# Performance work log

Measured on AMD Instinct MI355X. Metric: run time of the kernel, lower is better.

## Reference

```python
import jax, jax.numpy as jnp
import numpy as np

POOL_LEN = 2
POOL_SIZE = 4  # pool_len**2
NUM_ITERS = 3

def pool_grid(pool_size):
    # grid of relative positions inside the pooling block, row-major, centered at 0
    b = int(np.sqrt(pool_size))
    off = np.arange(b, dtype=np.float32) - (b - 1) / 2.0
    hh, ww = np.meshgrid(off, off, indexing='ij')
    return jnp.asarray(np.stack([hh.ravel(), ww.ravel()], -1))  # (pool_size, 2)

def posevec_to_rotmat(p):
    # p = (cos t, sin t) unit vector -> [[c,-s],[s,c]]
    x, y = p[..., 0], p[..., 1]
    return jnp.stack([jnp.stack([x, -y], -1), jnp.stack([y, x], -1)], -2)

def inverse_pose(p):
    return jnp.stack([p[..., 0], -p[..., 1]], -1)

def space_to_depth(x, b):
    # x: (B,H,W,D,P) -> (B,H/b,W/b,b*b*D,P), depth ordered (h_in_block, w_in_block, d)
    B, H, W, D, P = x.shape
    x = x.reshape(B, H // b, b, W // b, b, D, P).transpose(0, 1, 3, 2, 4, 5, 6)
    return x.reshape(B, H // b, W // b, b * b * D, P)

def capsule_forward(x, a, pose, alpha, beta, lin_w, lin_b, tg1_w, tg2_w):
    B, H, W, Cin = a.shape
    Cout = lin_w.shape[0]
    b, P = POOL_LEN, POOL_SIZE
    Hp, Wp = (H + 1) // b, (W + 1) // b
    a4 = space_to_depth(a[..., None], b)[..., 0].reshape(B, Hp, Wp, P, Cin)
    pose4 = space_to_depth(pose, b).reshape(B, Hp, Wp, P, Cin, 2)
    # mean_per_channel: sum over pool positions, normalize with zero-norm guard
    m = pose4.sum(3)                                            # (B,Hp,Wp,Cin,2)
    n = jnp.linalg.norm(m, axis=-1, keepdims=True)
    means = m / (n + (1.0 - jnp.sign(n)))
    # get_votes: rotate pool positions into the mean frame, generate per-pair thetas
    pp = pool_grid(P).reshape(1, 1, 1, P, 1, 2, 1)
    rot = posevec_to_rotmat(inverse_pose(means))[:, :, :, None]  # (B,Hp,Wp,1,Cin,2,2)
    tpos = jnp.matmul(rot, pp)                                   # (B,Hp,Wp,P,Cin,2,1)
    tpos = jax.lax.stop_gradient(tpos).reshape(-1, Cin * 2)      # detach(); (B*Hp*Wp*P, 2Cin)
    theta = (tpos @ tg1_w.T) @ tg2_w.T                           # (N, Cout*Cin)
    theta = theta.reshape(B, Hp, Wp, P, Cout, Cin).transpose(0, 1, 2, 4, 3, 5)
    s, c = jnp.sin(theta), jnp.cos(theta)
    g = jnp.stack([c, -s, s, c], -1).reshape(B, Hp, Wp, Cout, P, Cin, 2, 2)
    pm = posevec_to_rotmat(pose4[:, :, :, None])                 # (B,Hp,Wp,1,P,Cin,2,2)
    vote = jnp.matmul(pm, g)[..., 0].reshape(B, Hp, Wp, Cout, P * Cin, 2)

    def mean_fn(v, w):
        mu = (v * w[..., None]).sum(-2)                          # (B,Hp,Wp,Cout,2)
        msk = jnp.sign(jnp.abs(mu))                              # elementwise, as original
        return mu / (jnp.linalg.norm(mu, axis=-1, keepdims=True) + (1.0 - msk))

    def dist(p, v):
        return (1.0 - (p[..., None, :] * v).sum(-1)) / 2.0

    a_e = jnp.broadcast_to(a4.reshape(B, Hp, Wp, 1, P * Cin), (B, Hp, Wp, Cout, P * Cin))
    weight = a_e
    pose_o = mean_fn(vote, weight)
    for _ in range(NUM_ITERS):
        weight = (1.0 - dist(pose_o, vote)) * a_e
        pose_o = mean_fn(vote, weight)
    nd = (1.0 - dist(pose_o, vote)) * weight
    w_sum = jnp.sign(jnp.abs(weight)).sum(-1)
    msk = jnp.sign(jnp.abs(w_sum))
    nd = nd.sum(-1) / (w_sum + (1.0 - msk)) * msk
    agreement = jax.nn.sigmoid(alpha.reshape(1, 1, 1, -1) * nd + (beta.reshape(1, 1, 1, -1) - 1.0)) * msk
    # feature max-pool + linear
    xp = space_to_depth(x[..., None], b)[..., 0].reshape(B, Hp, Wp, P, Cin).max(-2)
    xp = xp.reshape(-1, Cin)
    x_out = xp @ lin_w.T + lin_b
    return x_out, agreement, pose_o, xp

def setup_inputs():
    key = jax.random.key(0)
    ks = jax.random.split(key, 8)
    B, H, W, Cin, Cout = 8, 32, 32, 32, 64
    x = jax.random.normal(ks[0], (B, H, W, Cin), jnp.float32)
    a = jax.random.uniform(ks[1], (B, H, W, Cin), jnp.float32)
    pose = jax.random.normal(ks[2], (B, H, W, Cin, 2), jnp.float32)
    pose = pose / jnp.linalg.norm(pose, axis=-1, keepdims=True)  # unit pose vectors
    alpha = jnp.ones((1,), jnp.float32)
    beta = jnp.ones((1,), jnp.float32)
    lin_w = jax.random.normal(ks[3], (Cout, Cin), jnp.float32) * 0.1
    lin_b = jax.random.normal(ks[4], (Cout,), jnp.float32) * 0.1
    tg1_w = jax.random.normal(ks[5], (32, 2 * Cin), jnp.float32) * 0.1
    tg2_w = jax.random.normal(ks[6], (Cout * Cin, 32), jnp.float32) * 0.1
    return {"x": x, "a": a, "pose": pose, "alpha": alpha, "beta": beta,
            "lin_w": lin_w, "lin_b": lin_b, "tg1_w": tg1_w, "tg2_w": tg2_w}

def reference(x, a, pose, alpha, beta, lin_w, lin_b, tg1_w, tg2_w):
    return capsule_forward(x, a, pose, alpha, beta, lin_w, lin_b, tg1_w, tg2_w)
```

## Files before the change

kernel.cpp:

```cpp
#include <hip/hip_runtime.h>
#include <math.h>

#define NSITE 2048

#define OFF_XOUT 0
#define OFF_AGR  (NSITE*64)
#define OFF_POSE (OFF_AGR + NSITE*64)
#define OFF_XP   (OFF_POSE + NSITE*128)

#define WS_META_OFF (NSITE*128)

__device__ __forceinline__ void norm2_guard(float x, float y, float* ox, float* oy) {
    const float n2  = x*x + y*y;
    const float inv = (n2 > 0.f) ? rsqrtf(n2) : 0.f;
    *ox = x*inv; *oy = y*inv;
}

__global__ __launch_bounds__(128) void capsA(
    const float* __restrict__ x, const float* __restrict__ a,
    const float* __restrict__ pose,
    const float* __restrict__ tg1, const float* __restrict__ lin_w,
    const float* __restrict__ lin_b, float* __restrict__ out,
    float* __restrict__ ws)
{
    const int s  = blockIdx.x;
    const int b  = s >> 8;
    const int hp = (s >> 4) & 15;
    const int wp = s & 15;
    const int t  = threadIdx.x;
    const int p  = t >> 5, ci = t & 31;
    const int dh = p >> 1, dw = p & 1;
    const int yy = 2*hp + dh, xx = 2*wp + dw;

    __shared__ float spx[128], spy[128], sxv[128], sav[128];
    __shared__ float smx[32],  smy[32],  sxp[32];
    __shared__ float stp[4*64];

    const int gidx = (((b*32 + yy)*32 + xx)*32 + ci);
    const float2 pv = ((const float2*)pose)[gidx];
    spx[t] = pv.x; spy[t] = pv.y;
    sxv[t] = x[gidx];
    sav[t] = a[gidx];
    __syncthreads();

    if (t < 32) {
        float mx = 0.f, my = 0.f, xm = -INFINITY, sa = 0.f, cnt = 0.f;
        #pragma unroll
        for (int q = 0; q < 4; q++) {
            mx += spx[q*32 + t];
            my += spy[q*32 + t];
            xm  = fmaxf(xm, sxv[q*32 + t]);
            const float av = sav[q*32 + t];
            sa += av;
            cnt += (av != 0.f) ? 1.f : 0.f;
        }
        const float n   = sqrtf(mx*mx + my*my);
        const float den = n + (n == 0.0f ? 1.0f : 0.0f);
        smx[t] = mx / den;
        smy[t] = my / den;
        sxp[t] = xm;
        out[OFF_XP + s*32 + t] = xm;
        #pragma unroll
        for (int m = 1; m <= 16; m <<= 1) {
            sa  += __shfl_xor(sa,  m, 64);
            cnt += __shfl_xor(cnt, m, 64);
        }
        if (t == 0) ((float2*)(ws + WS_META_OFF))[s] = make_float2(sa, cnt);
    }
    __syncthreads();

    {
        const float hh = (float)dh - 0.5f;
        const float ww = (float)dw - 0.5f;
        const float mx = smx[ci], my = smy[ci];
        stp[p*64 + 2*ci    ] =  mx*hh + my*ww;
        stp[p*64 + 2*ci + 1] = -my*hh + mx*ww;
    }
    __syncthreads();

    {
        const float* w = tg1 + ci*64;
        const float* v = stp + p*64;
        float acc = 0.f;
        #pragma unroll
        for (int k = 0; k < 64; k++) acc += w[k]*v[k];
        ws[s*128 + p*32 + ci] = acc;
    }

    if (t < 64) {
        float acc = lin_b[t];
        const float* w = lin_w + t*32;
        #pragma unroll
        for (int k = 0; k < 32; k++) acc += w[k]*sxp[k];
        out[OFF_XOUT + s*64 + t] = acc;
    }
}

__global__ __launch_bounds__(256) void capsB(
    const float* __restrict__ a, const float* __restrict__ pose,
    const float* __restrict__ tg2, const float* __restrict__ ws,
    const float* __restrict__ alpha, const float* __restrict__ beta,
    float* __restrict__ out)
{
    const int g    = blockIdx.x;
    const int sb   = blockIdx.y;
    const int tid  = threadIdx.x;
    const int wave = tid >> 6, lane = tid & 63;
    const int co   = g*8 + wave*2 + (lane >> 5);
    const int ci   = lane & 31;

    float4 r[8];
    {
        const float4* rp = (const float4*)(tg2 + (co*32 + ci)*32);
        #pragma unroll
        for (int k = 0; k < 8; ++k) r[k] = rp[k];
    }
    const float alp = alpha[0];
    const float bet = beta[0] - 1.0f;
    const float2* ws_meta = (const float2*)(ws + WS_META_OFF);

    const int s0 = sb*8;
    for (int s = s0; s < s0 + 8; ++s) {
        const float4* h4 = (const float4*)(ws + s*128);
        float th0 = 0.f, th1 = 0.f, th2 = 0.f, th3 = 0.f;
        #pragma unroll
        for (int k = 0; k < 8; ++k) {
            const float4 rk = r[k];
            const float4 ha = h4[k];
            const float4 hb = h4[8  + k];
            const float4 hc = h4[16 + k];
            const float4 hd = h4[24 + k];
            th0 += rk.x*ha.x + rk.y*ha.y + rk.z*ha.z + rk.w*ha.w;
            th1 += rk.x*hb.x + rk.y*hb.y + rk.z*hb.z + rk.w*hb.w;
            th2 += rk.x*hc.x + rk.y*hc.y + rk.z*hc.z + rk.w*hc.w;
            th3 += rk.x*hd.x + rk.y*hd.y + rk.z*hd.z + rk.w*hd.w;
        }
        const float th[4] = {th0, th1, th2, th3};

        const int b   = s >> 8, hpi = (s >> 4) & 15, wpi = s & 15;
        const int base = ((b*32 + 2*hpi)*32 + 2*wpi)*32 + ci;

        float Sx = 0.f, Sy = 0.f, Sxx = 0.f, Sxy = 0.f, Syy = 0.f;
        #pragma unroll
        for (int p = 0; p < 4; ++p) {
            const int idx = base + (p >> 1)*1024 + (p & 1)*32;
            const float2 pe = ((const float2*)pose)[idx];
            const float  av = a[idx];
            float sn, cs;
            __sincosf(th[p], &sn, &cs);
            const float vx = pe.x*cs - pe.y*sn;
            const float vy = pe.y*cs + pe.x*sn;
            const float ax = av*vx, ay = av*vy;
            Sx += ax; Sy += ay;
            Sxx += ax*vx; Sxy += ax*vy; Syy += ay*vy;
        }
        #pragma unroll
        for (int m = 1; m <= 16; m <<= 1) {
            Sx  += __shfl_xor(Sx,  m, 64);
            Sy  += __shfl_xor(Sy,  m, 64);
            Sxx += __shfl_xor(Sxx, m, 64);
            Sxy += __shfl_xor(Sxy, m, 64);
            Syy += __shfl_xor(Syy, m, 64);
        }

        float px, py;
        norm2_guard(Sx, Sy, &px, &py);
        float qx = px, qy = py;
        #pragma unroll
        for (int it = 0; it < 3; ++it) {
            qx = px; qy = py;
            const float mx = Sx + px*Sxx + py*Sxy;
            const float my = Sy + px*Sxy + py*Syy;
            norm2_guard(mx, my, &px, &py);
        }
        const float2 meta = ws_meta[s];
        const float nd_sum = 0.25f*(meta.x + (px + qx)*Sx + (py + qy)*Sy
                           + px*qx*Sxx + (px*qy + py*qx)*Sxy + py*qy*Syy);
        const float wsum = meta.y;
        const float msk  = (wsum != 0.f) ? 1.f : 0.f;
        const float nd   = nd_sum / (wsum + (1.f - msk)) * msk;
        const float z    = alp*nd + bet;
        const float agr  = msk / (1.f + __expf(-z));

        if ((lane & 31) == 0) {
            out[OFF_AGR  + s*64  + co]       = agr;
            out[OFF_POSE + s*128 + co*2]     = px;
            out[OFF_POSE + s*128 + co*2 + 1] = py;
        }
    }
}

extern "C" void kernel_launch(void* const* d_in, const int* in_sizes, int n_in,
                              void* d_out, int out_size, void* d_ws, size_t ws_size,
                              hipStream_t stream) {
    const float* x     = (const float*)d_in[0];
    const float* a     = (const float*)d_in[1];
    const float* pose  = (const float*)d_in[2];
    const float* alpha = (const float*)d_in[3];
    const float* beta  = (const float*)d_in[4];
    const float* lin_w = (const float*)d_in[5];
    const float* lin_b = (const float*)d_in[6];
    const float* tg1   = (const float*)d_in[7];
    const float* tg2   = (const float*)d_in[8];
    float* out = (float*)d_out;
    float* ws  = (float*)d_ws;

    capsA<<<NSITE, 128, 0, stream>>>(x, a, pose, tg1, lin_w, lin_b, out, ws);
    capsB<<<dim3(8, NSITE/8), 256, 0, stream>>>(a, pose, tg2, ws, alpha, beta, out);
}
```

Measured before the change: 147.4 us.

## Restructure capsA to one wave per site with shuffle reductions

```diff
diff --git a/kernel.cpp b/kernel.cpp
--- a/kernel.cpp
+++ b/kernel.cpp
@@ -16,83 +16,100 @@
     *ox = x*inv; *oy = y*inv;
 }
 
-__global__ __launch_bounds__(128) void capsA(
+__global__ __launch_bounds__(256) void capsA(
     const float* __restrict__ x, const float* __restrict__ a,
     const float* __restrict__ pose,
     const float* __restrict__ tg1, const float* __restrict__ lin_w,
     const float* __restrict__ lin_b, float* __restrict__ out,
     float* __restrict__ ws)
 {
-    const int s  = blockIdx.x;
-    const int b  = s >> 8;
-    const int hp = (s >> 4) & 15;
-    const int wp = s & 15;
-    const int t  = threadIdx.x;
-    const int p  = t >> 5, ci = t & 31;
-    const int dh = p >> 1, dw = p & 1;
-    const int yy = 2*hp + dh, xx = 2*wp + dw;
-
-    __shared__ float spx[128], spy[128], sxv[128], sav[128];
-    __shared__ float smx[32],  smy[32],  sxp[32];
-    __shared__ float stp[4*64];
-
-    const int gidx = (((b*32 + yy)*32 + xx)*32 + ci);
-    const float2 pv = ((const float2*)pose)[gidx];
-    spx[t] = pv.x; spy[t] = pv.y;
-    sxv[t] = x[gidx];
-    sav[t] = a[gidx];
+    const int wave = threadIdx.x >> 6, lane = threadIdx.x & 63;
+    const int s  = blockIdx.x*4 + wave;
+    const int b  = s >> 8, hp = (s >> 4) & 15, wp = s & 15;
+    const int ci = lane & 31, p0 = lane >> 5;
+
+    __shared__ float stp[4][4][64];
+    __shared__ float xps[4][32];
+
+    const int base = ((b*32 + 2*hp)*32 + 2*wp)*32 + ci;
+    const int i0 = base + p0*32;
+    const int i1 = base + 1024 + p0*32;
+    const float2 pe0 = ((const float2*)pose)[i0];
+    const float2 pe1 = ((const float2*)pose)[i1];
+    const float  x0  = x[i0], x1 = x[i1];
+    const float  a0  = a[i0], a1 = a[i1];
+
+    const float o0x = __shfl_xor(pe0.x, 32, 64);
+    const float o0y = __shfl_xor(pe0.y, 32, 64);
+    const float o1x = __shfl_xor(pe1.x, 32, 64);
+    const float o1y = __shfl_xor(pe1.y, 32, 64);
+    const bool first = (p0 == 0);
+    const float A0x = first ? pe0.x : o0x,  A1x = first ? o0x : pe0.x;
+    const float A2x = first ? pe1.x : o1x,  A3x = first ? o1x : pe1.x;
+    const float A0y = first ? pe0.y : o0y,  A1y = first ? o0y : pe0.y;
+    const float A2y = first ? pe1.y : o1y,  A3y = first ? o1y : pe1.y;
+    float mx = ((A0x + A1x) + A2x) + A3x;
+    float my = ((A0y + A1y) + A2y) + A3y;
+
+    float xm = fmaxf(x0, x1);
+    xm = fmaxf(xm, __shfl_xor(xm, 32, 64));
+    float sa  = a0 + a1;
+    float cnt = (a0 != 0.f ? 1.f : 0.f) + (a1 != 0.f ? 1.f : 0.f);
+    sa  += __shfl_xor(sa,  32, 64);
+    cnt += __shfl_xor(cnt, 32, 64);
+    #pragma unroll
+    for (int m = 1; m <= 16; m <<= 1) {
+        sa  += __shfl_xor(sa,  m, 64);
+        cnt += __shfl_xor(cnt, m, 64);
+    }
+    if (lane == 0) ((float2*)(ws + WS_META_OFF))[s] = make_float2(sa, cnt);
+    if (p0 == 0) {
+        out[OFF_XP + s*32 + ci] = xm;
+        xps[wave][ci] = xm;
+    }
+
+    {
+        const float n   = sqrtf(mx*mx + my*my);
+        const float den = n + (n == 0.f ? 1.f : 0.f);
+        mx /= den; my /= den;
+    }
+
+    {
+        const float ww_ = (float)p0 - 0.5f;
+        const float t0x = -0.5f*mx + my*ww_;
+        const float t0y =  0.5f*my + mx*ww_;
+        const float t1x =  0.5f*mx + my*ww_;
+        const float t1y = -0.5f*my + mx*ww_;
+        ((float2*)stp[wave][p0    ])[ci] = make_float2(t0x, t0y);
+        ((float2*)stp[wave][p0 + 2])[ci] = make_float2(t1x, t1y);
+    }
     __syncthreads();
 
-    if (t < 32) {
-        float mx = 0.f, my = 0.f, xm = -INFINITY, sa = 0.f, cnt = 0.f;
-        #pragma unroll
-        for (int q = 0; q < 4; q++) {
-            mx += spx[q*32 + t];
-            my += spy[q*32 + t];
-            xm  = fmaxf(xm, sxv[q*32 + t]);
-            const float av = sav[q*32 + t];
-            sa += av;
-            cnt += (av != 0.f) ? 1.f : 0.f;
-        }
-        const float n   = sqrtf(mx*mx + my*my);
-        const float den = n + (n == 0.0f ? 1.0f : 0.0f);
-        smx[t] = mx / den;
-        smy[t] = my / den;
-        sxp[t] = xm;
-        out[OFF_XP + s*32 + t] = xm;
-        #pragma unroll
-        for (int m = 1; m <= 16; m <<= 1) {
-            sa  += __shfl_xor(sa,  m, 64);
-            cnt += __shfl_xor(cnt, m, 64);
-        }
-        if (t == 0) ((float2*)(ws + WS_META_OFF))[s] = make_float2(sa, cnt);
-    }
-    __syncthreads();
-
-    {
-        const float hh = (float)dh - 0.5f;
-        const float ww = (float)dw - 0.5f;
-        const float mx = smx[ci], my = smy[ci];
-        stp[p*64 + 2*ci    ] =  mx*hh + my*ww;
-        stp[p*64 + 2*ci + 1] = -my*hh + mx*ww;
-    }
-    __syncthreads();
-
-    {
-        const float* w = tg1 + ci*64;
-        const float* v = stp + p*64;
-        float acc = 0.f;
-        #pragma unroll
-        for (int k = 0; k < 64; k++) acc += w[k]*v[k];
-        ws[s*128 + p*32 + ci] = acc;
-    }
-
-    if (t < 64) {
-        float acc = lin_b[t];
-        const float* w = lin_w + t*32;
-        #pragma unroll
-        for (int k = 0; k < 32; k++) acc += w[k]*sxp[k];
-        out[OFF_XOUT + s*64 + t] = acc;
+    {
+        const float4* w4 = (const float4*)(tg1 + ci*64);
+        const float4* r0 = (const float4*)stp[wave][p0];
+        const float4* r1 = (const float4*)stp[wave][p0 + 2];
+        float h0 = 0.f, h1 = 0.f;
+        #pragma unroll
+        for (int k = 0; k < 16; ++k) {
+            const float4 wv = w4[k], u = r0[k], v = r1[k];
+            h0 += wv.x*u.x + wv.y*u.y + wv.z*u.z + wv.w*u.w;
+            h1 += wv.x*v.x + wv.y*v.y + wv.z*v.z + wv.w*v.w;
+        }
+        ws[s*128 + p0*32 + ci]       = h0;
+        ws[s*128 + (p0 + 2)*32 + ci] = h1;
+    }
+
+    {
+        float acc = lin_b[lane];
+        const float4* lw = (const float4*)(lin_w + lane*32);
+        const float4* xv = (const float4*)xps[wave];
+        #pragma unroll
+        for (int k = 0; k < 8; ++k) {
+            const float4 wv = lw[k], u = xv[k];
+            acc += wv.x*u.x + wv.y*u.y + wv.z*u.z + wv.w*u.w;
+        }
+        out[OFF_XOUT + s*64 + lane] = acc;
     }
 }
 
@@ -205,6 +222,6 @@
     float* out = (float*)d_out;
     float* ws  = (float*)d_ws;
 
-    capsA<<<NSITE, 128, 0, stream>>>(x, a, pose, tg1, lin_w, lin_b, out, ws);
+    capsA<<<NSITE/4, 256, 0, stream>>>(x, a, pose, tg1, lin_w, lin_b, out, ws);
     capsB<<<dim3(8, NSITE/8), 256, 0, stream>>>(a, pose, tg2, ws, alpha, beta, out);
 }
```

Measured after the change: 144.4 us. -2.1%, faster.
